# Kernel tuning notes

Measured on AMD Instinct MI355X. Metric: run time of the kernel, lower is better.

Reference implementation:

```python
import jax, jax.numpy as jnp
import numpy as np
from jax import lax

DN = ('NHWC', 'HWIO', 'NHWC')
N_MEM = 2000  # memory slots
BN_EPS = 1e-3


def _conv(x, w, b):
    # tf.nn.conv2d stride 2, SAME, NHWC / HWIO
    return lax.conv_general_dilated(x, w, (2, 2), 'SAME', dimension_numbers=DN) + b


def _convt(x, w, b):
    # tf.nn.conv2d_transpose; w is TF layout [kh, kw, out_ch, in_ch]
    return lax.conv_transpose(x, w, (2, 2), 'SAME', dimension_numbers=DN,
                              transpose_kernel=True) + b


def _bn(x, g, b):
    # BatchNormalization(training=True): batch statistics over N,H,W
    m = jnp.mean(x, axis=(0, 1, 2))
    v = jnp.var(x, axis=(0, 1, 2))
    return g * (x - m) * lax.rsqrt(v + BN_EPS) + b


def setup_inputs() -> dict:
    key = jax.random.key(0)
    ks = iter(jax.random.split(key, 40))
    def gn(shape, s=0.05):
        return jax.random.normal(next(ks), shape, jnp.float32) * s
    inp = {'x': jax.random.uniform(next(ks), (16, 256, 256, 3), jnp.float32)}
    inp.update(
        w_e1=gn((1, 1, 3, 16)), b_e1=gn((16,)),
        g_bn1=jnp.ones(16, jnp.float32), be_bn1=jnp.zeros(16, jnp.float32),
        w_e2=gn((3, 3, 16, 32)), b_e2=gn((32,)),
        g_bn2=jnp.ones(32, jnp.float32), be_bn2=jnp.zeros(32, jnp.float32),
        w_e3=gn((3, 3, 32, 64)), b_e3=gn((64,)),
        g_bn3=jnp.ones(64, jnp.float32), be_bn3=jnp.zeros(64, jnp.float32),
        w_mem=gn((1, 1, N_MEM, 64)),
        w_d1=gn((3, 3, 32, 64)), b_d1=gn((32,)),
        g_bnt1=jnp.ones(32, jnp.float32), be_bnt1=jnp.zeros(32, jnp.float32),
        w_d2=gn((3, 3, 16, 32)), b_d2=gn((16,)),
        g_bnt2=jnp.ones(16, jnp.float32), be_bnt2=jnp.zeros(16, jnp.float32),
        w_d3=gn((3, 3, 3, 16)), b_d3=gn((3,)),
    )
    return inp


def reference(x, w_e1, b_e1, g_bn1, be_bn1, w_e2, b_e2, g_bn2, be_bn2,
              w_e3, b_e3, g_bn3, be_bn3, w_mem,
              w_d1, b_d1, g_bnt1, be_bnt1, w_d2, b_d2, g_bnt2, be_bnt2,
              w_d3, b_d3):
    # ---- encode ----
    h = jax.nn.relu(_bn(_conv(x, w_e1, b_e1), g_bn1, be_bn1))   # [B,128,128,16]
    h = jax.nn.relu(_bn(_conv(h, w_e2, b_e2), g_bn2, be_bn2))   # [B,64,64,32]
    z = jax.nn.relu(_bn(_conv(h, w_e3, b_e3), g_bn3, be_bn3))   # [B,32,32,64]
    # ---- memory addressing ----
    mem = w_mem[0, 0]                                            # [N, 64]
    num = jnp.einsum('bhwc,nc->bhwn', z, mem)
    den = jnp.einsum('bhwc,nc->bhwn', z * z, mem * mem)
    att = jax.nn.softmax((num + 1e-12) / (den + 1e-12), axis=-1)  # [B,32,32,N]
    d = att - 1.0 / N_MEM                                        # hard shrinkage
    renorm = jnp.clip(jax.nn.relu(d) * att / (jnp.abs(d) + 1e-12),
                      1e-12, 1.0 - 1e-12)
    z_hat = jnp.einsum('bhwn,nc->bhwc', renorm, mem)             # [B,32,32,64]
    # ---- decode ----
    t = jax.nn.relu(_bn(_convt(z_hat, w_d1, b_d1), g_bnt1, be_bnt1))  # [B,64,64,32]
    t = jax.nn.relu(_bn(_convt(t, w_d2, b_d2), g_bnt2, be_bnt2))      # [B,128,128,16]
    x_hat = jnp.clip(_convt(t, w_d3, b_d3), 1e-12, 1.0 - 1e-12)       # [B,256,256,3]
    return x_hat
```

## Files before the change

### kernel.cpp

```cpp
#include <hip/hip_runtime.h>
#include <math.h>

typedef __bf16 bf16x8 __attribute__((ext_vector_type(8)));
typedef __bf16 bf16x4 __attribute__((ext_vector_type(4)));
typedef float  f32x16 __attribute__((ext_vector_type(16)));

static __device__ __forceinline__ f32x16 zero16() {
  f32x16 v;
  #pragma unroll
  for (int i = 0; i < 16; ++i) v[i] = 0.f;
  return v;
}
static __device__ __forceinline__ unsigned int bfbits(__bf16 b) {
  return (unsigned int)__builtin_bit_cast(unsigned short, b);
}
static __device__ __forceinline__ bf16x8 mk8(unsigned int a, unsigned int b,
                                             unsigned int c, unsigned int d) {
  uint4 t; t.x = a; t.y = b; t.z = c; t.w = d;
  return __builtin_bit_cast(bf16x8, t);
}

__global__ __launch_bounds__(256) void k_conv1(const float* __restrict__ x,
    const float* __restrict__ w, const float* __restrict__ b, float* __restrict__ y,
    float* __restrict__ partials) {
  int t = blockIdx.x*256 + threadIdx.x;
  int ox = t & 127, oy = (t >> 7) & 127, bb = t >> 14;
  const float* xp = x + ((size_t)((bb*256 + 2*oy)*256 + 2*ox))*3;
  float x0 = xp[0], x1 = xp[1], x2 = xp[2];
  float4 rg[4];
  float4* yp = (float4*)(y + (size_t)t*16);
  #pragma unroll
  for (int g = 0; g < 4; ++g) {
    float4 r;
    r.x = b[g*4+0] + x0*w[g*4+0] + x1*w[16+g*4+0] + x2*w[32+g*4+0];
    r.y = b[g*4+1] + x0*w[g*4+1] + x1*w[16+g*4+1] + x2*w[32+g*4+1];
    r.z = b[g*4+2] + x0*w[g*4+2] + x1*w[16+g*4+2] + x2*w[32+g*4+2];
    r.w = b[g*4+3] + x0*w[g*4+3] + x1*w[16+g*4+3] + x2*w[32+g*4+3];
    rg[g] = r;
    yp[g] = r;
  }
  float4 s4[4], q4[4];
  #pragma unroll
  for (int g=0; g<4; ++g) {
    s4[g] = rg[g];
    q4[g] = make_float4(rg[g].x*rg[g].x, rg[g].y*rg[g].y, rg[g].z*rg[g].z, rg[g].w*rg[g].w);
  }
  #pragma unroll
  for (int off=1; off<64; off<<=1) {
    #pragma unroll
    for (int g=0; g<4; ++g) {
      s4[g].x += __shfl_xor(s4[g].x, off); s4[g].y += __shfl_xor(s4[g].y, off);
      s4[g].z += __shfl_xor(s4[g].z, off); s4[g].w += __shfl_xor(s4[g].w, off);
      q4[g].x += __shfl_xor(q4[g].x, off); q4[g].y += __shfl_xor(q4[g].y, off);
      q4[g].z += __shfl_xor(q4[g].z, off); q4[g].w += __shfl_xor(q4[g].w, off);
    }
  }
  __shared__ float red[4][32];
  int wv = threadIdx.x >> 6, lane = threadIdx.x & 63;
  if (lane == 0) {
    #pragma unroll
    for (int g=0; g<4; ++g) {
      *(float4*)&red[wv][g*4]      = s4[g];
      *(float4*)&red[wv][16 + g*4] = q4[g];
    }
  }
  __syncthreads();
  if (threadIdx.x < 32)
    partials[(size_t)blockIdx.x*32 + threadIdx.x] =
      red[0][threadIdx.x]+red[1][threadIdx.x]+red[2][threadIdx.x]+red[3][threadIdx.x];
}

template<int C,int CSPLIT>
__global__ __launch_bounds__(256) void k_finalize2(const float* __restrict__ partials, int nblk,
    double inv_n, const float* __restrict__ g, const float* __restrict__ be, float* __restrict__ ss) {
  const int COUTT = C/CSPLIT;
  const int NSTAT = 2*C;
  const int PER = 256/NSTAT;
  __shared__ double red[256];
  int tid = threadIdx.x;
  int st = tid % NSTAT, sub = tid / NSTAT;
  int c = st % C, kind = st / C;
  int cq = c / COUTT, j = c % COUTT;
  int nb = nblk / CSPLIT;
  double acc = 0.0;
  #pragma unroll 4
  for (int i = sub; i < nb; i += PER) {
    int bq = cq + i*CSPLIT;
    acc += (double)partials[(size_t)bq*2*COUTT + kind*COUTT + j];
  }
  red[tid] = acc;
  __syncthreads();
  for (int off = PER>>1; off > 0; off >>= 1) {
    if (sub < off) red[tid] += red[tid + off*NSTAT];
    __syncthreads();
  }
  if (tid < C) {
    double mean = red[tid]*inv_n;
    double var  = red[C+tid]*inv_n - mean*mean;
    float scale = g[tid] * rsqrtf((float)var + 1e-3f);
    float shift = be[tid] - (float)mean*scale;
    ss[tid] = scale; ss[C+tid] = shift;
  }
}

template<int CIN,int COUT,int CSPLIT,int HIN,int HOUT,bool BN>
__global__ __launch_bounds__(256) void k_conv_bn(const float* __restrict__ in,
    const float* __restrict__ w, const float* __restrict__ bias,
    const float* __restrict__ ss, float* __restrict__ y, float* __restrict__ partials) {
  const int COUTT = COUT/CSPLIT;
  const int NW4 = COUTT/4;
  __shared__ float4 wlds[9*CIN*NW4];
  int bid = blockIdx.x;
  int cq  = bid % CSPLIT;
  int pxb = bid / CSPLIT;
  int c0  = cq*COUTT;
  for (int e = threadIdx.x; e < 9*CIN*NW4; e += 256) {
    int r = e / NW4, cg = e % NW4;
    wlds[e] = *(const float4*)(w + (size_t)r*COUT + c0 + cg*4);
  }
  __syncthreads();
  int t0 = pxb*256 + threadIdx.x;
  float4 acc[NW4];
  #pragma unroll
  for (int g=0; g<NW4; ++g) acc[g] = *(const float4*)(bias + c0 + g*4);
  int ox = t0 % HOUT, oy = (t0/HOUT) % HOUT, bb = t0/(HOUT*HOUT);
  #pragma unroll 1
  for (int dy=0; dy<3; ++dy) {
    #pragma unroll 1
    for (int dx=0; dx<3; ++dx) {
      int tap = dy*3+dx;
      int iy = 2*oy + dy, ix = 2*ox + dx;
      if (iy < HIN && ix < HIN) {
        const float* bp = in + ((size_t)(bb*HIN + iy)*HIN + ix)*CIN;
        #pragma unroll
        for (int ci4=0; ci4<CIN/4; ++ci4) {
          float4 v = *(const float4*)(bp + ci4*4);
          if (BN) {
            float4 sc = *(const float4*)(ss + ci4*4);
            float4 sh = *(const float4*)(ss + CIN + ci4*4);
            v.x = fmaxf(0.f, fmaf(v.x, sc.x, sh.x));
            v.y = fmaxf(0.f, fmaf(v.y, sc.y, sh.y));
            v.z = fmaxf(0.f, fmaf(v.z, sc.z, sh.z));
            v.w = fmaxf(0.f, fmaf(v.w, sc.w, sh.w));
          }
          float va[4] = {v.x, v.y, v.z, v.w};
          #pragma unroll
          for (int k=0;k<4;++k) {
            float vk = va[k];
            #pragma unroll
            for (int g=0; g<NW4; ++g) {
              float4 w4 = wlds[(tap*CIN + ci4*4 + k)*NW4 + g];
              acc[g].x = fmaf(vk, w4.x, acc[g].x);
              acc[g].y = fmaf(vk, w4.y, acc[g].y);
              acc[g].z = fmaf(vk, w4.z, acc[g].z);
              acc[g].w = fmaf(vk, w4.w, acc[g].w);
            }
          }
        }
      }
    }
  }
  float4* yp = (float4*)(y + (size_t)t0*COUT + c0);
  #pragma unroll
  for (int g=0;g<NW4;++g) yp[g] = acc[g];
  float4 s4[NW4], q4[NW4];
  #pragma unroll
  for (int g=0; g<NW4; ++g) {
    s4[g] = acc[g];
    q4[g] = make_float4(acc[g].x*acc[g].x, acc[g].y*acc[g].y,
                        acc[g].z*acc[g].z, acc[g].w*acc[g].w);
  }
  #pragma unroll
  for (int off=1; off<64; off<<=1) {
    #pragma unroll
    for (int g=0; g<NW4; ++g) {
      s4[g].x += __shfl_xor(s4[g].x, off); s4[g].y += __shfl_xor(s4[g].y, off);
      s4[g].z += __shfl_xor(s4[g].z, off); s4[g].w += __shfl_xor(s4[g].w, off);
      q4[g].x += __shfl_xor(q4[g].x, off); q4[g].y += __shfl_xor(q4[g].y, off);
      q4[g].z += __shfl_xor(q4[g].z, off); q4[g].w += __shfl_xor(q4[g].w, off);
    }
  }
  __shared__ float red[4][2*COUTT];
  int wv = threadIdx.x >> 6, lane = threadIdx.x & 63;
  if (lane == 0) {
    #pragma unroll
    for (int g=0; g<NW4; ++g) {
      *(float4*)&red[wv][g*4]         = s4[g];
      *(float4*)&red[wv][COUTT + g*4] = q4[g];
    }
  }
  __syncthreads();
  if (threadIdx.x < 2*COUTT)
    partials[(size_t)bid*2*COUTT + threadIdx.x] =
      red[0][threadIdx.x]+red[1][threadIdx.x]+red[2][threadIdx.x]+red[3][threadIdx.x];
}


__global__ __launch_bounds__(256) void k_prep_z(const float* __restrict__ y3,
    const float* __restrict__ ss,
    __bf16* __restrict__ ZH, __bf16* __restrict__ ZL,
    __bf16* __restrict__ Z2H, __bf16* __restrict__ Z2L) {
  int t = blockIdx.x*256 + threadIdx.x;
  float4 v = ((const float4*)y3)[t];
  int c0 = (t*4) & 63;
  float4 sc = *(const float4*)(ss + c0);
  float4 sh = *(const float4*)(ss + 64 + c0);
  float vv[4];
  vv[0] = fmaxf(0.f, fmaf(v.x, sc.x, sh.x));
  vv[1] = fmaxf(0.f, fmaf(v.y, sc.y, sh.y));
  vv[2] = fmaxf(0.f, fmaf(v.z, sc.z, sh.z));
  vv[3] = fmaxf(0.f, fmaf(v.w, sc.w, sh.w));
  bf16x4 h, l, h2, l2;
  #pragma unroll
  for (int i=0;i<4;++i) {
    float f = vv[i];
    __bf16 hb = (__bf16)f;
    h[i] = hb; l[i] = (__bf16)(f - (float)hb);
    float q = f*f;
    __bf16 qb = (__bf16)q;
    h2[i] = qb; l2[i] = (__bf16)(q - (float)qb);
  }
  ((bf16x4*)ZH)[t] = h;  ((bf16x4*)ZL)[t] = l;
  ((bf16x4*)Z2H)[t] = h2; ((bf16x4*)Z2L)[t] = l2;
}

__global__ __launch_bounds__(256) void k_prep_m(const float* __restrict__ mem,
    __bf16* __restrict__ MH, __bf16* __restrict__ ML,
    __bf16* __restrict__ M2H, __bf16* __restrict__ M2L,
    __bf16* __restrict__ MHT) {
  int t = blockIdx.x*256 + threadIdx.x;
  int n = t >> 4, c0 = (t & 15)*4;
  float4 v = make_float4(0.f,0.f,0.f,0.f);
  if (n < 2000) v = *(const float4*)(mem + (size_t)n*64 + c0);
  float vv[4] = {v.x, v.y, v.z, v.w};
  bf16x4 h, l, h2, l2;
  #pragma unroll
  for (int i=0;i<4;++i) {
    float f = vv[i];
    __bf16 hb = (__bf16)f;
    h[i] = hb; l[i] = (__bf16)(f - (float)hb);
    float q = f*f;
    __bf16 qb = (__bf16)q;
    h2[i] = qb; l2[i] = (__bf16)(q - (float)qb);
  }
  *(bf16x4*)(MH  + (size_t)n*64 + c0) = h;
  *(bf16x4*)(ML  + (size_t)n*64 + c0) = l;
  *(bf16x4*)(M2H + (size_t)n*64 + c0) = h2;
  *(bf16x4*)(M2L + (size_t)n*64 + c0) = l2;
  #pragma unroll
  for (int i=0;i<4;++i) {
    MHT[(size_t)(c0+i)*2048 + n] = h[i];
  }
}

__global__ __launch_bounds__(256) void k_pass1(
    const __bf16* __restrict__ ZH, const __bf16* __restrict__ ZL,
    const __bf16* __restrict__ Z2H, const __bf16* __restrict__ Z2L,
    const __bf16* __restrict__ MH, const __bf16* __restrict__ ML,
    const __bf16* __restrict__ M2H, const __bf16* __restrict__ M2L,
    __bf16* __restrict__ U, float* __restrict__ MT,
    float* __restrict__ partM, float* __restrict__ partS) {
  int chunk = blockIdx.x & 15, pbg = blockIdx.x >> 4;
  int wave = threadIdx.x >> 6, lane = threadIdx.x & 63;
  int p0 = pbg*128 + wave*32;
  int col = lane & 31, hi = lane >> 5;
  bf16x8 bzh[4], bzl[4], b2h[4], b2l[4];
  size_t zoff = (size_t)(p0 + col)*64 + hi*8;
  #pragma unroll
  for (int ks=0;ks<4;++ks) {
    bzh[ks] = *(const bf16x8*)(ZH  + zoff + ks*16);
    bzl[ks] = *(const bf16x8*)(ZL  + zoff + ks*16);
    b2h[ks] = *(const bf16x8*)(Z2H + zoff + ks*16);
    b2l[ks] = *(const bf16x8*)(Z2L + zoff + ks*16);
  }
  float tmaxv[4], ssumv[4];
  int nbase = chunk*128;
  #pragma unroll
  for (int t=0; t<4; ++t) {
    int n0 = nbase + t*32;
    size_t arow = (size_t)(n0 + col)*64 + hi*8;
    f32x16 num = zero16(), den = zero16();
    #pragma unroll
    for (int ks=0;ks<4;++ks) {
      bf16x8 amh = *(const bf16x8*)(MH + arow + ks*16);
      bf16x8 aml = *(const bf16x8*)(ML + arow + ks*16);
      num = __builtin_amdgcn_mfma_f32_32x32x16_bf16(amh, bzh[ks], num, 0,0,0);
      num = __builtin_amdgcn_mfma_f32_32x32x16_bf16(amh, bzl[ks], num, 0,0,0);
      num = __builtin_amdgcn_mfma_f32_32x32x16_bf16(aml, bzh[ks], num, 0,0,0);
      bf16x8 a2h = *(const bf16x8*)(M2H + arow + ks*16);
      bf16x8 a2l = *(const bf16x8*)(M2L + arow + ks*16);
      den = __builtin_amdgcn_mfma_f32_32x32x16_bf16(a2h, b2h[ks], den, 0,0,0);
      den = __builtin_amdgcn_mfma_f32_32x32x16_bf16(a2h, b2l[ks], den, 0,0,0);
      den = __builtin_amdgcn_mfma_f32_32x32x16_bf16(a2l, b2h[ks], den, 0,0,0);
    }
    bool maskt = (n0 + 32 > 2000);
    float sv[16];
    float tmax = -3.4e38f;
    #pragma unroll
    for (int r=0;r<16;++r) {
      float s = (num[r] + 1e-12f) * __builtin_amdgcn_rcpf(den[r] + 1e-12f);
      if (maskt) {
        int nn = n0 + (r&3) + 8*(r>>2) + 4*hi;
        if (nn >= 2000) s = -3.4e38f;
      }
      sv[r] = s;
      tmax = fmaxf(tmax, s);
    }
    float ssum = 0.f;
    unsigned int up[8];
    #pragma unroll
    for (int j=0;j<8;++j) {
      float u0 = __expf(sv[2*j]   - tmax);
      float u1 = __expf(sv[2*j+1] - tmax);
      ssum += u0; ssum += u1;
      up[j] = bfbits((__bf16)u0) | (bfbits((__bf16)u1) << 16);
    }
    size_t idx = (size_t)((chunk*4 + t)*16384 + p0 + col)*2 + hi;
    uint4 st0; st0.x = up[0]; st0.y = up[1]; st0.z = up[2]; st0.w = up[3];
    uint4 st1; st1.x = up[4]; st1.y = up[5]; st1.z = up[6]; st1.w = up[7];
    *(uint4*)(U + idx*16)     = st0;
    *(uint4*)(U + idx*16 + 8) = st1;
    MT[idx] = tmax;
    tmaxv[t] = tmax; ssumv[t] = ssum;
  }
  float m = fmaxf(fmaxf(tmaxv[0], tmaxv[1]), fmaxf(tmaxv[2], tmaxv[3]));
  float S = ssumv[0]*__expf(tmaxv[0]-m) + ssumv[1]*__expf(tmaxv[1]-m)
          + ssumv[2]*__expf(tmaxv[2]-m) + ssumv[3]*__expf(tmaxv[3]-m);
  float mo = __shfl_xor(m, 32);
  float So = __shfl_xor(S, 32);
  float mf = fmaxf(m, mo);
  float Sf = S*__expf(m - mf) + So*__expf(mo - mf);
  if (lane < 32) {
    int p = p0 + col;
    partM[chunk*16384 + p] = mf;
    partS[chunk*16384 + p] = Sf;
  }
}

__global__ __launch_bounds__(256) void k_pass2(
    const __bf16* __restrict__ U, const float* __restrict__ MT,
    const __bf16* __restrict__ MHT,
    const float* __restrict__ partM, const float* __restrict__ partS,
    float* __restrict__ Gz) {
  __shared__ float zl[4][32][68];
  int pbg = blockIdx.x;
  int wave = threadIdx.x >> 6, lane = threadIdx.x & 63;
  int p0 = pbg*32;
  int col = lane & 31, hi = lane >> 5;
  int p = p0 + col;
  float pmv[16];
  float Mp = -3.4e38f;
  #pragma unroll
  for (int c=0;c<16;++c) { pmv[c] = partM[c*16384 + p]; Mp = fmaxf(Mp, pmv[c]); }
  float Ssum = 0.f;
  #pragma unroll
  for (int c=0;c<16;++c) Ssum += partS[c*16384 + p] * __expf(pmv[c] - Mp);
  float CM  = Mp + __logf(Ssum);
  float thr = CM - 7.6009025f;
  f32x16 za0 = zero16(), za1 = zero16();
  #pragma unroll 2
  for (int t=0; t<16; ++t) {
    int tg = wave*16 + t;
    int n0 = tg*32;
    size_t idx = (size_t)(tg*16384 + p)*2 + hi;
    uint4 a = *(const uint4*)(U + idx*16);
    uint4 b = *(const uint4*)(U + idx*16 + 8);
    float mt = MT[idx];
    float scale = __expf(mt - CM);
    float thru  = __expf(thr - mt);
    unsigned int ua[8] = {a.x,a.y,a.z,a.w,b.x,b.y,b.z,b.w};
    unsigned int qh[8];
    #pragma unroll
    for (int j=0;j<8;++j) {
      float u0 = __builtin_bit_cast(float, ua[j] << 16);
      float u1 = __builtin_bit_cast(float, ua[j] & 0xffff0000u);
      float r0 = (u0 > thru) ? u0*scale : 0.f;
      float r1 = (u1 > thru) ? u1*scale : 0.f;
      qh[j] = bfbits((__bf16)r0) | (bfbits((__bf16)r1) << 16);
    }
    unsigned int qhp[8];
    #pragma unroll
    for (int i=0;i<8;++i) qhp[i] = (unsigned int)__shfl_xor((int)qh[i], 32);
    bf16x8 f1h = hi ? mk8(qhp[2],qhp[3],qh[2],qh[3]) : mk8(qh[0],qh[1],qhp[0],qhp[1]);
    bf16x8 f2h = hi ? mk8(qhp[6],qhp[7],qh[6],qh[7]) : mk8(qh[4],qh[5],qhp[4],qhp[5]);
    #pragma unroll
    for (int kh=0; kh<2; ++kh) {
      bf16x8 fh = kh ? f2h : f1h;
      size_t bofs = (size_t)col*2048 + n0 + kh*16 + hi*8;
      bf16x8 bmh0 = *(const bf16x8*)(MHT + bofs);
      bf16x8 bmh1 = *(const bf16x8*)(MHT + bofs + (size_t)32*2048);
      za0 = __builtin_amdgcn_mfma_f32_32x32x16_bf16(fh, bmh0, za0, 0,0,0);
      za1 = __builtin_amdgcn_mfma_f32_32x32x16_bf16(fh, bmh1, za1, 0,0,0);
    }
  }
  #pragma unroll
  for (int r=0;r<16;++r) {
    int prow = (r&3) + 8*(r>>2) + 4*hi;
    zl[wave][prow][col]      = za0[r];
    zl[wave][prow][col + 32] = za1[r];
  }
  __syncthreads();
  int tp = threadIdx.x >> 3;
  int tc = (threadIdx.x & 7) * 8;
  float4 s0 = make_float4(0.f,0.f,0.f,0.f);
  float4 s1 = make_float4(0.f,0.f,0.f,0.f);
  #pragma unroll
  for (int w2=0; w2<4; ++w2) {
    float4 a0 = *(const float4*)&zl[w2][tp][tc];
    float4 a1 = *(const float4*)&zl[w2][tp][tc+4];
    s0.x += a0.x; s0.y += a0.y; s0.z += a0.z; s0.w += a0.w;
    s1.x += a1.x; s1.y += a1.y; s1.z += a1.z; s1.w += a1.w;
  }
  float* gp = Gz + (size_t)(p0 + tp)*64 + tc;
  *(float4*)gp       = s0;
  *(float4*)(gp + 4) = s1;
}

template<int CIN,int COUT,int CSPLIT,int HIN,bool BN>
__global__ __launch_bounds__(256) void k_convt_bn(const float* __restrict__ in,
    const float* __restrict__ w, const float* __restrict__ bias,
    const float* __restrict__ ss, float* __restrict__ y, float* __restrict__ partials) {
  const int COUTT = COUT/CSPLIT;
  const int HOUT = 2*HIN;
  __shared__ float4 wlds[4*COUTT*(CIN/4)];
  int bid = blockIdx.x;
  int cq = bid % CSPLIT; int rest = bid / CSPLIT;
  int cls = rest % 4;    int pxb = rest / 4;
  int pm = cls >> 1, pn = cls & 1;
  int c0 = cq*COUTT;
  int NTI = (pm == 0) ? 2 : 1;
  int NTJ = (pn == 0) ? 2 : 1;
  int NT = NTI*NTJ;
  for (int e = threadIdx.x; e < NT*COUTT*(CIN/4); e += 256) {
    int tl = e / (COUTT*(CIN/4));
    int rem = e % (COUTT*(CIN/4));
    int cc = rem / (CIN/4), ci4 = rem % (CIN/4);
    int ki = pm + 2*(tl / NTJ), kj = pn + 2*(tl % NTJ);
    wlds[e] = *(const float4*)(w + ((size_t)(ki*3+kj)*COUT + c0 + cc)*CIN + ci4*4);
  }
  __syncthreads();
  int t0 = pxb*256 + threadIdx.x;
  float acc[COUTT];
  #pragma unroll
  for (int cc=0;cc<COUTT;++cc) acc[cc] = bias[c0+cc];
  int nx = t0 % HIN, my = (t0/HIN) % HIN, bb = t0/(HIN*HIN);
  #pragma unroll 1
  for (int ti=0; ti<NTI; ++ti) {
    #pragma unroll 1
    for (int tj=0; tj<NTJ; ++tj) {
      int tl = ti*NTJ + tj;
      int i = my - ti, j = nx - tj;
      if (i >= 0 && j >= 0) {
        const float* bp = in + ((size_t)(bb*HIN + i)*HIN + j)*CIN;
        #pragma unroll
        for (int ci4=0; ci4<CIN/4; ++ci4) {
          float4 v = *(const float4*)(bp + ci4*4);
          if (BN) {
            float4 sc = *(const float4*)(ss + ci4*4);
            float4 sh = *(const float4*)(ss + CIN + ci4*4);
            v.x = fmaxf(0.f, fmaf(v.x, sc.x, sh.x));
            v.y = fmaxf(0.f, fmaf(v.y, sc.y, sh.y));
            v.z = fmaxf(0.f, fmaf(v.z, sc.z, sh.z));
            v.w = fmaxf(0.f, fmaf(v.w, sc.w, sh.w));
          }
          #pragma unroll
          for (int cc=0;cc<COUTT;++cc) {
            float4 w4 = wlds[(tl*COUTT + cc)*(CIN/4) + ci4];
            float a = acc[cc];
            a = fmaf(v.x, w4.x, a);
            a = fmaf(v.y, w4.y, a);
            a = fmaf(v.z, w4.z, a);
            a = fmaf(v.w, w4.w, a);
            acc[cc] = a;
          }
        }
      }
    }
  }
  int m = 2*my + pm, n = 2*nx + pn;
  float* yp = y + ((size_t)(bb*HOUT + m)*HOUT + n)*COUT + c0;
  #pragma unroll
  for (int g=0;g<COUTT/4;++g)
    ((float4*)yp)[g] = make_float4(acc[g*4], acc[g*4+1], acc[g*4+2], acc[g*4+3]);
  float s[COUTT], q[COUTT];
  #pragma unroll
  for (int cc=0;cc<COUTT;++cc) { s[cc] = acc[cc]; q[cc] = acc[cc]*acc[cc]; }
  #pragma unroll
  for (int off=1; off<64; off<<=1) {
    #pragma unroll
    for (int cc=0;cc<COUTT;++cc) {
      s[cc] += __shfl_xor(s[cc], off);
      q[cc] += __shfl_xor(q[cc], off);
    }
  }
  __shared__ float red[4][2*COUTT];
  int wv = threadIdx.x >> 6, lane = threadIdx.x & 63;
  if (lane == 0) {
    #pragma unroll
    for (int cc=0;cc<COUTT;++cc) { red[wv][cc] = s[cc]; red[wv][COUTT+cc] = q[cc]; }
  }
  __syncthreads();
  if (threadIdx.x < 2*COUTT)
    partials[(size_t)bid*2*COUTT + threadIdx.x] =
      red[0][threadIdx.x]+red[1][threadIdx.x]+red[2][threadIdx.x]+red[3][threadIdx.x];
}

__global__ __launch_bounds__(256) void k_convt_final(const float* __restrict__ in,
    const float* __restrict__ w, const float* __restrict__ bias,
    const float* __restrict__ ss, float* __restrict__ out) {
  const int CIN=16, HIN=128, HOUT=256;
  __shared__ float4 wlds[4*3*4];
  int cls = blockIdx.x & 3;
  int pxb = blockIdx.x >> 2;
  int pm = cls >> 1, pn = cls & 1;
  int NTI = (pm == 0) ? 2 : 1;
  int NTJ = (pn == 0) ? 2 : 1;
  int NT = NTI*NTJ;
  if (threadIdx.x < NT*3*4) {
    int e = threadIdx.x;
    int tl = e / 12, rem = e % 12;
    int c = rem / 4, ci4 = rem % 4;
    int ki = pm + 2*(tl / NTJ), kj = pn + 2*(tl % NTJ);
    wlds[e] = *(const float4*)(w + ((size_t)(ki*3+kj)*3 + c)*CIN + ci4*4);
  }
  __syncthreads();
  int t = pxb*256 + threadIdx.x;
  int nx = t % HIN, my = (t/HIN) % HIN, bb = t/(HIN*HIN);
  float a0 = bias[0], a1 = bias[1], a2 = bias[2];
  #pragma unroll 1
  for (int ti=0; ti<NTI; ++ti) {
    #pragma unroll 1
    for (int tj=0; tj<NTJ; ++tj) {
      int tl = ti*NTJ + tj;
      int i = my - ti, j = nx - tj;
      if (i >= 0 && j >= 0) {
        const float* bp = in + ((size_t)(bb*HIN + i)*HIN + j)*CIN;
        #pragma unroll
        for (int ci4=0; ci4<4; ++ci4) {
          float4 v = *(const float4*)(bp + ci4*4);
          float4 sc = *(const float4*)(ss + ci4*4);
          float4 sh = *(const float4*)(ss + CIN + ci4*4);
          v.x = fmaxf(0.f, fmaf(v.x, sc.x, sh.x));
          v.y = fmaxf(0.f, fmaf(v.y, sc.y, sh.y));
          v.z = fmaxf(0.f, fmaf(v.z, sc.z, sh.z));
          v.w = fmaxf(0.f, fmaf(v.w, sc.w, sh.w));
          float4 w0 = wlds[(tl*3 + 0)*4 + ci4];
          float4 w1 = wlds[(tl*3 + 1)*4 + ci4];
          float4 w2 = wlds[(tl*3 + 2)*4 + ci4];
          a0 = fmaf(v.x, w0.x, a0); a0 = fmaf(v.y, w0.y, a0);
          a0 = fmaf(v.z, w0.z, a0); a0 = fmaf(v.w, w0.w, a0);
          a1 = fmaf(v.x, w1.x, a1); a1 = fmaf(v.y, w1.y, a1);
          a1 = fmaf(v.z, w1.z, a1); a1 = fmaf(v.w, w1.w, a1);
          a2 = fmaf(v.x, w2.x, a2); a2 = fmaf(v.y, w2.y, a2);
          a2 = fmaf(v.z, w2.z, a2); a2 = fmaf(v.w, w2.w, a2);
        }
      }
    }
  }
  int m = 2*my + pm, n = 2*nx + pn;
  float* op = out + ((size_t)(bb*HOUT + m)*HOUT + n)*3;
  op[0] = fminf(fmaxf(a0, 1e-12f), 1.0f);
  op[1] = fminf(fmaxf(a1, 1e-12f), 1.0f);
  op[2] = fminf(fmaxf(a2, 1e-12f), 1.0f);
}

extern "C" void kernel_launch(void* const* d_in, const int* in_sizes, int n_in,
                              void* d_out, int out_size, void* d_ws, size_t ws_size,
                              hipStream_t stream) {
  const float* x    = (const float*)d_in[0];
  const float* w_e1 = (const float*)d_in[1];
  const float* b_e1 = (const float*)d_in[2];
  const float* g1   = (const float*)d_in[3];
  const float* be1  = (const float*)d_in[4];
  const float* w_e2 = (const float*)d_in[5];
  const float* b_e2 = (const float*)d_in[6];
  const float* g2   = (const float*)d_in[7];
  const float* be2  = (const float*)d_in[8];
  const float* w_e3 = (const float*)d_in[9];
  const float* b_e3 = (const float*)d_in[10];
  const float* g3   = (const float*)d_in[11];
  const float* be3  = (const float*)d_in[12];
  const float* wmem = (const float*)d_in[13];
  const float* w_d1 = (const float*)d_in[14];
  const float* b_d1 = (const float*)d_in[15];
  const float* gt1  = (const float*)d_in[16];
  const float* bet1 = (const float*)d_in[17];
  const float* w_d2 = (const float*)d_in[18];
  const float* b_d2 = (const float*)d_in[19];
  const float* gt2  = (const float*)d_in[20];
  const float* bet2 = (const float*)d_in[21];
  const float* w_d3 = (const float*)d_in[22];
  const float* b_d3 = (const float*)d_in[23];
  float* out = (float*)d_out;

  float* ws = (float*)d_ws;
  __bf16* U  = (__bf16*)ws;
  float* A   = ws;
  float* Cc  = ws + 4194304;
  float* Gz  = ws + 16777216;
  float* E   = Gz + 1048576 + 8388608;
  float* bfbase = E + 1048576;
  __bf16* ZH  = (__bf16*)bfbase;
  __bf16* ZL  = ZH  + 16384*64;
  __bf16* Z2H = ZL  + 16384*64;
  __bf16* Z2L = Z2H + 16384*64;
  __bf16* MH  = Z2L + 16384*64;
  __bf16* ML  = MH  + 2048*64;
  __bf16* M2H = ML  + 2048*64;
  __bf16* M2L = M2H + 2048*64;
  __bf16* MHT = M2L + 2048*64;
  __bf16* MLT = MHT + 64*2048;
  float* PT   = (float*)(MLT + 64*2048);
  float* SS   = PT + 131072;
  float* PM   = SS + 256;
  float* PS   = PM + 262144;
  float* MT   = PS + 262144;
  (void)ws_size; (void)in_sizes; (void)n_in; (void)out_size;

  k_conv1<<<1024,256,0,stream>>>(x, w_e1, b_e1, A, PT);
  k_finalize2<16,1><<<1,256,0,stream>>>(PT, 1024, 1.0/262144.0, g1, be1, SS);
  k_conv_bn<16,32,2,128,64,true><<<512,256,0,stream>>>(A, w_e2, b_e2, SS, Cc, PT);
  k_finalize2<32,2><<<1,256,0,stream>>>(PT, 512, 1.0/65536.0, g2, be2, SS);
  k_conv_bn<32,64,8,64,32,true><<<512,256,0,stream>>>(Cc, w_e3, b_e3, SS, E, PT);
  k_finalize2<64,8><<<1,256,0,stream>>>(PT, 512, 1.0/16384.0, g3, be3, SS);
  k_prep_m<<<128,256,0,stream>>>(wmem, MH, ML, M2H, M2L, MHT);
  k_prep_z<<<1024,256,0,stream>>>(E, SS, ZH, ZL, Z2H, Z2L);
  k_pass1<<<2048,256,0,stream>>>(ZH, ZL, Z2H, Z2L, MH, ML, M2H, M2L, U, MT, PM, PS);
  k_pass2<<<512,256,0,stream>>>(U, MT, MHT, PM, PS, Gz);
  k_convt_bn<64,32,2,32,false><<<512,256,0,stream>>>(Gz, w_d1, b_d1, nullptr, Cc, PT);
  k_finalize2<32,2><<<1,256,0,stream>>>(PT, 512, 1.0/65536.0, gt1, bet1, SS);
  k_convt_bn<32,16,1,64,true><<<1024,256,0,stream>>>(Cc, w_d2, b_d2, SS, A, PT);
  k_finalize2<16,1><<<1,256,0,stream>>>(PT, 1024, 1.0/262144.0, gt2, bet2, SS);
  k_convt_final<<<4096,256,0,stream>>>(A, w_d3, b_d3, SS, out);
}
```

Measured before the change: 340.4 us.

## Fold BN-statistics finalize into consumer conv kernels and merge prep kernels

Removes four single-block k_finalize2 launches. Each consuming conv or convt block now reduces the producer's per-block partials itself, in double precision in shared memory, to get its BN scale and shift. The memory and z prep kernels are merged into one launch. This cuts launch count and the serialised 1-block gaps between stages. In exchange every block redundantly reads all the partials (up to 1024x32 floats) and does extra reductions and syncs. Partial buffers are split per stage so producers do not overwrite inputs still being read.

```diff
diff --git a/kernel.cpp b/kernel.cpp
--- a/kernel.cpp
+++ b/kernel.cpp
@@ -18,6 +18,38 @@
                                              unsigned int c, unsigned int d) {
   uint4 t; t.x = a; t.y = b; t.z = c; t.w = d;
   return __builtin_bit_cast(bf16x8, t);
+}
+
+template<int C, int CSPLITP>
+static __device__ __forceinline__ void block_finalize(const float* __restrict__ partials,
+    int nblk, double inv_n, const float* __restrict__ g, const float* __restrict__ be,
+    float* __restrict__ ssl, double* __restrict__ red) {
+  const int COUTT = C/CSPLITP;
+  const int NSTAT = 2*C;
+  const int PER = 256/NSTAT;
+  int tid = threadIdx.x;
+  int st = tid % NSTAT, sub = tid / NSTAT;
+  int c = st % C, kind = st / C;
+  int cq = c / COUTT, j = c % COUTT;
+  int nb = nblk / CSPLITP;
+  double acc = 0.0;
+  #pragma unroll 4
+  for (int i = sub; i < nb; i += PER)
+    acc += (double)partials[(size_t)(cq + i*CSPLITP)*2*COUTT + kind*COUTT + j];
+  red[tid] = acc;
+  __syncthreads();
+  for (int off = PER>>1; off > 0; off >>= 1) {
+    if (sub < off) red[tid] += red[tid + off*NSTAT];
+    __syncthreads();
+  }
+  if (tid < C) {
+    double mean = red[tid]*inv_n;
+    double var  = red[C+tid]*inv_n - mean*mean;
+    float scale = g[tid] * rsqrtf((float)var + 1e-3f);
+    ssl[tid] = scale;
+    ssl[C+tid] = be[tid] - (float)mean*scale;
+  }
+  __syncthreads();
 }
 
 __global__ __launch_bounds__(256) void k_conv1(const float* __restrict__ x,
@@ -103,13 +135,16 @@
   }
 }
 
-template<int CIN,int COUT,int CSPLIT,int HIN,int HOUT,bool BN>
+template<int CIN,int COUT,int CSPLIT,int HIN,int HOUT,int CP,int CSPLITP>
 __global__ __launch_bounds__(256) void k_conv_bn(const float* __restrict__ in,
     const float* __restrict__ w, const float* __restrict__ bias,
-    const float* __restrict__ ss, float* __restrict__ y, float* __restrict__ partials) {
+    const float* __restrict__ pin, const float* __restrict__ g, const float* __restrict__ be,
+    double inv_n, int nblk, float* __restrict__ y, float* __restrict__ partials) {
   const int COUTT = COUT/CSPLIT;
   const int NW4 = COUTT/4;
   __shared__ float4 wlds[9*CIN*NW4];
+  __shared__ double fred[256];
+  __shared__ __align__(16) float ssl[2*CIN];
   int bid = blockIdx.x;
   int cq  = bid % CSPLIT;
   int pxb = bid / CSPLIT;
@@ -118,11 +153,11 @@
     int r = e / NW4, cg = e % NW4;
     wlds[e] = *(const float4*)(w + (size_t)r*COUT + c0 + cg*4);
   }
-  __syncthreads();
+  block_finalize<CP,CSPLITP>(pin, nblk, inv_n, g, be, ssl, fred);
   int t0 = pxb*256 + threadIdx.x;
   float4 acc[NW4];
   #pragma unroll
-  for (int g=0; g<NW4; ++g) acc[g] = *(const float4*)(bias + c0 + g*4);
+  for (int gg=0; gg<NW4; ++gg) acc[gg] = *(const float4*)(bias + c0 + gg*4);
   int ox = t0 % HOUT, oy = (t0/HOUT) % HOUT, bb = t0/(HOUT*HOUT);
   #pragma unroll 1
   for (int dy=0; dy<3; ++dy) {
@@ -135,25 +170,23 @@
         #pragma unroll
         for (int ci4=0; ci4<CIN/4; ++ci4) {
           float4 v = *(const float4*)(bp + ci4*4);
-          if (BN) {
-            float4 sc = *(const float4*)(ss + ci4*4);
-            float4 sh = *(const float4*)(ss + CIN + ci4*4);
-            v.x = fmaxf(0.f, fmaf(v.x, sc.x, sh.x));
-            v.y = fmaxf(0.f, fmaf(v.y, sc.y, sh.y));
-            v.z = fmaxf(0.f, fmaf(v.z, sc.z, sh.z));
-            v.w = fmaxf(0.f, fmaf(v.w, sc.w, sh.w));
-          }
+          float4 sc = *(const float4*)(ssl + ci4*4);
+          float4 sh = *(const float4*)(ssl + CIN + ci4*4);
+          v.x = fmaxf(0.f, fmaf(v.x, sc.x, sh.x));
+          v.y = fmaxf(0.f, fmaf(v.y, sc.y, sh.y));
+          v.z = fmaxf(0.f, fmaf(v.z, sc.z, sh.z));
+          v.w = fmaxf(0.f, fmaf(v.w, sc.w, sh.w));
           float va[4] = {v.x, v.y, v.z, v.w};
           #pragma unroll
           for (int k=0;k<4;++k) {
             float vk = va[k];
             #pragma unroll
-            for (int g=0; g<NW4; ++g) {
-              float4 w4 = wlds[(tap*CIN + ci4*4 + k)*NW4 + g];
-              acc[g].x = fmaf(vk, w4.x, acc[g].x);
-              acc[g].y = fmaf(vk, w4.y, acc[g].y);
-              acc[g].z = fmaf(vk, w4.z, acc[g].z);
-              acc[g].w = fmaf(vk, w4.w, acc[g].w);
+            for (int gg=0; gg<NW4; ++gg) {
+              float4 w4 = wlds[(tap*CIN + ci4*4 + k)*NW4 + gg];
+              acc[gg].x = fmaf(vk, w4.x, acc[gg].x);
+              acc[gg].y = fmaf(vk, w4.y, acc[gg].y);
+              acc[gg].z = fmaf(vk, w4.z, acc[gg].z);
+              acc[gg].w = fmaf(vk, w4.w, acc[gg].w);
             }
           }
         }
@@ -162,94 +195,96 @@
   }
   float4* yp = (float4*)(y + (size_t)t0*COUT + c0);
   #pragma unroll
-  for (int g=0;g<NW4;++g) yp[g] = acc[g];
+  for (int gg=0;gg<NW4;++gg) yp[gg] = acc[gg];
   float4 s4[NW4], q4[NW4];
   #pragma unroll
-  for (int g=0; g<NW4; ++g) {
-    s4[g] = acc[g];
-    q4[g] = make_float4(acc[g].x*acc[g].x, acc[g].y*acc[g].y,
-                        acc[g].z*acc[g].z, acc[g].w*acc[g].w);
+  for (int gg=0; gg<NW4; ++gg) {
+    s4[gg] = acc[gg];
+    q4[gg] = make_float4(acc[gg].x*acc[gg].x, acc[gg].y*acc[gg].y,
+                         acc[gg].z*acc[gg].z, acc[gg].w*acc[gg].w);
   }
   #pragma unroll
   for (int off=1; off<64; off<<=1) {
     #pragma unroll
-    for (int g=0; g<NW4; ++g) {
-      s4[g].x += __shfl_xor(s4[g].x, off); s4[g].y += __shfl_xor(s4[g].y, off);
-      s4[g].z += __shfl_xor(s4[g].z, off); s4[g].w += __shfl_xor(s4[g].w, off);
-      q4[g].x += __shfl_xor(q4[g].x, off); q4[g].y += __shfl_xor(q4[g].y, off);
-      q4[g].z += __shfl_xor(q4[g].z, off); q4[g].w += __shfl_xor(q4[g].w, off);
-    }
-  }
-  __shared__ float red[4][2*COUTT];
+    for (int gg=0; gg<NW4; ++gg) {
+      s4[gg].x += __shfl_xor(s4[gg].x, off); s4[gg].y += __shfl_xor(s4[gg].y, off);
+      s4[gg].z += __shfl_xor(s4[gg].z, off); s4[gg].w += __shfl_xor(s4[gg].w, off);
+      q4[gg].x += __shfl_xor(q4[gg].x, off); q4[gg].y += __shfl_xor(q4[gg].y, off);
+      q4[gg].z += __shfl_xor(q4[gg].z, off); q4[gg].w += __shfl_xor(q4[gg].w, off);
+    }
+  }
+  __shared__ float red2[4][2*COUTT];
   int wv = threadIdx.x >> 6, lane = threadIdx.x & 63;
+  __syncthreads();
   if (lane == 0) {
     #pragma unroll
-    for (int g=0; g<NW4; ++g) {
-      *(float4*)&red[wv][g*4]         = s4[g];
-      *(float4*)&red[wv][COUTT + g*4] = q4[g];
+    for (int gg=0; gg<NW4; ++gg) {
+      *(float4*)&red2[wv][gg*4]         = s4[gg];
+      *(float4*)&red2[wv][COUTT + gg*4] = q4[gg];
     }
   }
   __syncthreads();
   if (threadIdx.x < 2*COUTT)
     partials[(size_t)bid*2*COUTT + threadIdx.x] =
-      red[0][threadIdx.x]+red[1][threadIdx.x]+red[2][threadIdx.x]+red[3][threadIdx.x];
-}
-
-
-__global__ __launch_bounds__(256) void k_prep_z(const float* __restrict__ y3,
-    const float* __restrict__ ss,
+      red2[0][threadIdx.x]+red2[1][threadIdx.x]+red2[2][threadIdx.x]+red2[3][threadIdx.x];
+}
+
+
+__global__ __launch_bounds__(256) void k_prep_mz(const float* __restrict__ mem,
+    const float* __restrict__ y3, const float* __restrict__ pin,
+    const float* __restrict__ g, const float* __restrict__ be,
+    __bf16* __restrict__ MH, __bf16* __restrict__ ML,
+    __bf16* __restrict__ M2H, __bf16* __restrict__ M2L, __bf16* __restrict__ MHT,
     __bf16* __restrict__ ZH, __bf16* __restrict__ ZL,
     __bf16* __restrict__ Z2H, __bf16* __restrict__ Z2L) {
-  int t = blockIdx.x*256 + threadIdx.x;
-  float4 v = ((const float4*)y3)[t];
-  int c0 = (t*4) & 63;
-  float4 sc = *(const float4*)(ss + c0);
-  float4 sh = *(const float4*)(ss + 64 + c0);
-  float vv[4];
-  vv[0] = fmaxf(0.f, fmaf(v.x, sc.x, sh.x));
-  vv[1] = fmaxf(0.f, fmaf(v.y, sc.y, sh.y));
-  vv[2] = fmaxf(0.f, fmaf(v.z, sc.z, sh.z));
-  vv[3] = fmaxf(0.f, fmaf(v.w, sc.w, sh.w));
-  bf16x4 h, l, h2, l2;
-  #pragma unroll
-  for (int i=0;i<4;++i) {
-    float f = vv[i];
-    __bf16 hb = (__bf16)f;
-    h[i] = hb; l[i] = (__bf16)(f - (float)hb);
-    float q = f*f;
-    __bf16 qb = (__bf16)q;
-    h2[i] = qb; l2[i] = (__bf16)(q - (float)qb);
-  }
-  ((bf16x4*)ZH)[t] = h;  ((bf16x4*)ZL)[t] = l;
-  ((bf16x4*)Z2H)[t] = h2; ((bf16x4*)Z2L)[t] = l2;
-}
-
-__global__ __launch_bounds__(256) void k_prep_m(const float* __restrict__ mem,
-    __bf16* __restrict__ MH, __bf16* __restrict__ ML,
-    __bf16* __restrict__ M2H, __bf16* __restrict__ M2L,
-    __bf16* __restrict__ MHT) {
-  int t = blockIdx.x*256 + threadIdx.x;
-  int n = t >> 4, c0 = (t & 15)*4;
-  float4 v = make_float4(0.f,0.f,0.f,0.f);
-  if (n < 2000) v = *(const float4*)(mem + (size_t)n*64 + c0);
-  float vv[4] = {v.x, v.y, v.z, v.w};
-  bf16x4 h, l, h2, l2;
-  #pragma unroll
-  for (int i=0;i<4;++i) {
-    float f = vv[i];
-    __bf16 hb = (__bf16)f;
-    h[i] = hb; l[i] = (__bf16)(f - (float)hb);
-    float q = f*f;
-    __bf16 qb = (__bf16)q;
-    h2[i] = qb; l2[i] = (__bf16)(q - (float)qb);
-  }
-  *(bf16x4*)(MH  + (size_t)n*64 + c0) = h;
-  *(bf16x4*)(ML  + (size_t)n*64 + c0) = l;
-  *(bf16x4*)(M2H + (size_t)n*64 + c0) = h2;
-  *(bf16x4*)(M2L + (size_t)n*64 + c0) = l2;
-  #pragma unroll
-  for (int i=0;i<4;++i) {
-    MHT[(size_t)(c0+i)*2048 + n] = h[i];
+  __shared__ double fred[256];
+  __shared__ __align__(16) float ssl[128];
+  if (blockIdx.x < 128) {
+    int t = blockIdx.x*256 + threadIdx.x;
+    int n = t >> 4, c0 = (t & 15)*4;
+    float4 v = make_float4(0.f,0.f,0.f,0.f);
+    if (n < 2000) v = *(const float4*)(mem + (size_t)n*64 + c0);
+    float vv[4] = {v.x, v.y, v.z, v.w};
+    bf16x4 h, l, h2, l2;
+    #pragma unroll
+    for (int i=0;i<4;++i) {
+      float f = vv[i];
+      __bf16 hb = (__bf16)f;
+      h[i] = hb; l[i] = (__bf16)(f - (float)hb);
+      float q = f*f;
+      __bf16 qb = (__bf16)q;
+      h2[i] = qb; l2[i] = (__bf16)(q - (float)qb);
+    }
+    *(bf16x4*)(MH  + (size_t)n*64 + c0) = h;
+    *(bf16x4*)(ML  + (size_t)n*64 + c0) = l;
+    *(bf16x4*)(M2H + (size_t)n*64 + c0) = h2;
+    *(bf16x4*)(M2L + (size_t)n*64 + c0) = l2;
+    #pragma unroll
+    for (int i=0;i<4;++i) MHT[(size_t)(c0+i)*2048 + n] = h[i];
+  } else {
+    block_finalize<64,8>(pin, 512, 1.0/16384.0, g, be, ssl, fred);
+    int t = (blockIdx.x - 128)*256 + threadIdx.x;
+    float4 v = ((const float4*)y3)[t];
+    int c0 = (t*4) & 63;
+    float4 sc = *(const float4*)(ssl + c0);
+    float4 sh = *(const float4*)(ssl + 64 + c0);
+    float vv[4];
+    vv[0] = fmaxf(0.f, fmaf(v.x, sc.x, sh.x));
+    vv[1] = fmaxf(0.f, fmaf(v.y, sc.y, sh.y));
+    vv[2] = fmaxf(0.f, fmaf(v.z, sc.z, sh.z));
+    vv[3] = fmaxf(0.f, fmaf(v.w, sc.w, sh.w));
+    bf16x4 h, l, h2, l2;
+    #pragma unroll
+    for (int i=0;i<4;++i) {
+      float f = vv[i];
+      __bf16 hb = (__bf16)f;
+      h[i] = hb; l[i] = (__bf16)(f - (float)hb);
+      float q = f*f;
+      __bf16 qb = (__bf16)q;
+      h2[i] = qb; l2[i] = (__bf16)(q - (float)qb);
+    }
+    ((bf16x4*)ZH)[t] = h;  ((bf16x4*)ZL)[t] = l;
+    ((bf16x4*)Z2H)[t] = h2; ((bf16x4*)Z2L)[t] = l2;
   }
 }
 
@@ -416,13 +451,16 @@
   *(float4*)(gp + 4) = s1;
 }
 
-template<int CIN,int COUT,int CSPLIT,int HIN,bool BN>
+template<int CIN,int COUT,int CSPLIT,int HIN,bool BN,int CP,int CSPLITP>
 __global__ __launch_bounds__(256) void k_convt_bn(const float* __restrict__ in,
     const float* __restrict__ w, const float* __restrict__ bias,
-    const float* __restrict__ ss, float* __restrict__ y, float* __restrict__ partials) {
+    const float* __restrict__ pin, const float* __restrict__ g, const float* __restrict__ be,
+    double inv_n, int nblk, float* __restrict__ y, float* __restrict__ partials) {
   const int COUTT = COUT/CSPLIT;
   const int HOUT = 2*HIN;
   __shared__ float4 wlds[4*COUTT*(CIN/4)];
+  __shared__ double fred[256];
+  __shared__ __align__(16) float ssl[2*CIN];
   int bid = blockIdx.x;
   int cq = bid % CSPLIT; int rest = bid / CSPLIT;
   int cls = rest % 4;    int pxb = rest / 4;
@@ -438,7 +476,11 @@
     int ki = pm + 2*(tl / NTJ), kj = pn + 2*(tl % NTJ);
     wlds[e] = *(const float4*)(w + ((size_t)(ki*3+kj)*COUT + c0 + cc)*CIN + ci4*4);
   }
-  __syncthreads();
+  if constexpr (BN) {
+    block_finalize<CP,CSPLITP>(pin, nblk, inv_n, g, be, ssl, fred);
+  } else {
+    __syncthreads();
+  }
   int t0 = pxb*256 + threadIdx.x;
   float acc[COUTT];
   #pragma unroll
@@ -456,8 +498,8 @@
         for (int ci4=0; ci4<CIN/4; ++ci4) {
           float4 v = *(const float4*)(bp + ci4*4);
           if (BN) {
-            float4 sc = *(const float4*)(ss + ci4*4);
-            float4 sh = *(const float4*)(ss + CIN + ci4*4);
+            float4 sc = *(const float4*)(ssl + ci4*4);
+            float4 sh = *(const float4*)(ssl + CIN + ci4*4);
             v.x = fmaxf(0.f, fmaf(v.x, sc.x, sh.x));
             v.y = fmaxf(0.f, fmaf(v.y, sc.y, sh.y));
             v.z = fmaxf(0.f, fmaf(v.z, sc.z, sh.z));
@@ -480,8 +522,8 @@
   int m = 2*my + pm, n = 2*nx + pn;
   float* yp = y + ((size_t)(bb*HOUT + m)*HOUT + n)*COUT + c0;
   #pragma unroll
-  for (int g=0;g<COUTT/4;++g)
-    ((float4*)yp)[g] = make_float4(acc[g*4], acc[g*4+1], acc[g*4+2], acc[g*4+3]);
+  for (int gg=0;gg<COUTT/4;++gg)
+    ((float4*)yp)[gg] = make_float4(acc[gg*4], acc[gg*4+1], acc[gg*4+2], acc[gg*4+3]);
   float s[COUTT], q[COUTT];
   #pragma unroll
   for (int cc=0;cc<COUTT;++cc) { s[cc] = acc[cc]; q[cc] = acc[cc]*acc[cc]; }
@@ -493,16 +535,17 @@
       q[cc] += __shfl_xor(q[cc], off);
     }
   }
-  __shared__ float red[4][2*COUTT];
+  __shared__ float red2[4][2*COUTT];
   int wv = threadIdx.x >> 6, lane = threadIdx.x & 63;
+  __syncthreads();
   if (lane == 0) {
     #pragma unroll
-    for (int cc=0;cc<COUTT;++cc) { red[wv][cc] = s[cc]; red[wv][COUTT+cc] = q[cc]; }
+    for (int cc=0;cc<COUTT;++cc) { red2[wv][cc] = s[cc]; red2[wv][COUTT+cc] = q[cc]; }
   }
   __syncthreads();
   if (threadIdx.x < 2*COUTT)
     partials[(size_t)bid*2*COUTT + threadIdx.x] =
-      red[0][threadIdx.x]+red[1][threadIdx.x]+red[2][threadIdx.x]+red[3][threadIdx.x];
+      red2[0][threadIdx.x]+red2[1][threadIdx.x]+red2[2][threadIdx.x]+red2[3][threadIdx.x];
 }
 
 __global__ __launch_bounds__(256) void k_convt_final(const float* __restrict__ in,
@@ -610,26 +653,31 @@
   __bf16* M2L = M2H + 2048*64;
   __bf16* MHT = M2L + 2048*64;
   __bf16* MLT = MHT + 64*2048;
-  float* PT   = (float*)(MLT + 64*2048);
-  float* SS   = PT + 131072;
+  float* PTb  = (float*)(MLT + 64*2048);
+  float* PT1  = PTb;
+  float* PT2  = PT1 + 32768;
+  float* PT3  = PT2 + 16384;
+  float* PTd1 = PT3 + 8192;
+  float* PTd2 = PTd1 + 16384;
+  float* SS   = PTb + 131072;
   float* PM   = SS + 256;
   float* PS   = PM + 262144;
   float* MT   = PS + 262144;
   (void)ws_size; (void)in_sizes; (void)n_in; (void)out_size;
 
-  k_conv1<<<1024,256,0,stream>>>(x, w_e1, b_e1, A, PT);
-  k_finalize2<16,1><<<1,256,0,stream>>>(PT, 1024, 1.0/262144.0, g1, be1, SS);
-  k_conv_bn<16,32,2,128,64,true><<<512,256,0,stream>>>(A, w_e2, b_e2, SS, Cc, PT);
-  k_finalize2<32,2><<<1,256,0,stream>>>(PT, 512, 1.0/65536.0, g2, be2, SS);
-  k_conv_bn<32,64,8,64,32,true><<<512,256,0,stream>>>(Cc, w_e3, b_e3, SS, E, PT);
-  k_finalize2<64,8><<<1,256,0,stream>>>(PT, 512, 1.0/16384.0, g3, be3, SS);
-  k_prep_m<<<128,256,0,stream>>>(wmem, MH, ML, M2H, M2L, MHT);
-  k_prep_z<<<1024,256,0,stream>>>(E, SS, ZH, ZL, Z2H, Z2L);
+  k_conv1<<<1024,256,0,stream>>>(x, w_e1, b_e1, A, PT1);
+  k_conv_bn<16,32,2,128,64,16,1><<<512,256,0,stream>>>(
+      A, w_e2, b_e2, PT1, g1, be1, 1.0/262144.0, 1024, Cc, PT2);
+  k_conv_bn<32,64,8,64,32,32,2><<<512,256,0,stream>>>(
+      Cc, w_e3, b_e3, PT2, g2, be2, 1.0/65536.0, 512, E, PT3);
+  k_prep_mz<<<1152,256,0,stream>>>(wmem, E, PT3, g3, be3,
+      MH, ML, M2H, M2L, MHT, ZH, ZL, Z2H, Z2L);
   k_pass1<<<2048,256,0,stream>>>(ZH, ZL, Z2H, Z2L, MH, ML, M2H, M2L, U, MT, PM, PS);
   k_pass2<<<512,256,0,stream>>>(U, MT, MHT, PM, PS, Gz);
-  k_convt_bn<64,32,2,32,false><<<512,256,0,stream>>>(Gz, w_d1, b_d1, nullptr, Cc, PT);
-  k_finalize2<32,2><<<1,256,0,stream>>>(PT, 512, 1.0/65536.0, gt1, bet1, SS);
-  k_convt_bn<32,16,1,64,true><<<1024,256,0,stream>>>(Cc, w_d2, b_d2, SS, A, PT);
-  k_finalize2<16,1><<<1,256,0,stream>>>(PT, 1024, 1.0/262144.0, gt2, bet2, SS);
+  k_convt_bn<64,32,2,32,false,16,1><<<512,256,0,stream>>>(
+      Gz, w_d1, b_d1, nullptr, nullptr, nullptr, 0.0, 0, Cc, PTd1);
+  k_convt_bn<32,16,1,64,true,32,2><<<1024,256,0,stream>>>(
+      Cc, w_d2, b_d2, PTd1, gt1, bet1, 1.0/65536.0, 512, A, PTd2);
+  k_finalize2<16,1><<<1,256,0,stream>>>(PTd2, 1024, 1.0/262144.0, gt2, bet2, SS);
   k_convt_final<<<4096,256,0,stream>>>(A, w_d3, b_d3, SS, out);
 }
```

After: 363.2 us. 6.7% more time.
